# Kernel optimization log

Hardware: AMD Instinct MI355X
Metric: run time of the kernel (lower is better)

## Reference

```python
import jax, jax.numpy as jnp
import numpy as np

IN_FEATURES = 4096
OUT_FEATURES = 8192
LUT_SIZE = 65536  # 256 * 256 two-level codebook


def setup_inputs() -> dict:
    key = jax.random.key(0)
    k_x, k_b, k_f, k_s, k_l = jax.random.split(key, 5)
    x = jax.random.normal(k_x, (2, 256, IN_FEATURES), dtype=jnp.float32)
    base_idx = jax.random.randint(k_b, (OUT_FEATURES, IN_FEATURES), 0, 256, dtype=jnp.int32)
    fine_idx = jax.random.randint(k_f, (OUT_FEATURES, IN_FEATURES), 0, 256, dtype=jnp.int32)
    scale = jax.random.uniform(k_s, (OUT_FEATURES, 1), dtype=jnp.float32)
    lut = jax.random.normal(k_l, (LUT_SIZE,), dtype=jnp.float32)
    return {"x": x, "base_idx": base_idx, "fine_idx": fine_idx, "scale": scale, "lut": lut}


def reference(x, base_idx, fine_idx, scale, lut):
    # Two-level LUT dequant: combined 16-bit index = base*256 + fine
    combined_idx = base_idx * 256 + fine_idx              # [out, in] int32
    weights = lut[combined_idx] * scale                   # [out, in] fp32, per-row scale
    # F.linear(x, weights) == x @ weights.T
    return jnp.einsum('bsi,oi->bso', x, weights)
```

## Files before the change

kernel.cpp:

```cpp
#include <hip/hip_runtime.h>

typedef unsigned short ushort_t;
typedef unsigned int   uint32;
typedef __attribute__((ext_vector_type(8)))  short short8;
typedef __attribute__((ext_vector_type(4)))  float floatx4;
typedef __attribute__((ext_vector_type(16))) float floatx16;

#define IN_F   4096
#define OUT_F  8192
#define M_TOT  512

__device__ __forceinline__ ushort_t f2bf(float f) {
    uint32 u = __builtin_bit_cast(uint32, f);
    u += 0x7FFFu + ((u >> 16) & 1u);
    return (ushort_t)(u >> 16);
}
__device__ __forceinline__ uint32 pack2bf(float a, float b) {
    return (uint32)f2bf(a) | ((uint32)f2bf(b) << 16);
}

__global__ void cvt_x_kernel(const float* __restrict__ x, ushort_t* __restrict__ xb) {
    int i = (blockIdx.x * 256 + threadIdx.x) * 8;
    float4 v0 = *(const float4*)(x + i);
    float4 v1 = *(const float4*)(x + i + 4);
    short8 s;
    s[0] = (short)f2bf(v0.x); s[1] = (short)f2bf(v0.y);
    s[2] = (short)f2bf(v0.z); s[3] = (short)f2bf(v0.w);
    s[4] = (short)f2bf(v1.x); s[5] = (short)f2bf(v1.y);
    s[6] = (short)f2bf(v1.z); s[7] = (short)f2bf(v1.w);
    *(short8*)(xb + i) = s;
}

__global__ __launch_bounds__(1024, 4)
void dequant_kernel(const int* __restrict__ base_idx, const int* __restrict__ fine_idx,
                    const float* __restrict__ lut, ushort_t* __restrict__ wq)
{
    __shared__ ushort_t sh_lut[65536];
    const int tid = threadIdx.x;
    for (int i = tid * 4; i < 65536; i += 1024 * 4) {
        float4 v = *(const float4*)(lut + i);
        *(uint32*)&sh_lut[i]     = pack2bf(v.x, v.y);
        *(uint32*)&sh_lut[i + 2] = pack2bf(v.z, v.w);
    }

    const int row   = blockIdx.x * 32 + (tid >> 5);
    const int kbase = blockIdx.y * 2048 + (tid & 31) * 4;
    const int* bp = base_idx + (size_t)row * IN_F + kbase;
    const int* fp = fine_idx + (size_t)row * IN_F + kbase;
    ushort_t*  op = wq       + (size_t)row * IN_F + kbase;

    int4 cb[2][4], cf[2][4];
#pragma unroll
    for (int u = 0; u < 4; ++u) {
        cb[0][u] = *(const int4*)(bp + u * 128);
        cf[0][u] = *(const int4*)(fp + u * 128);
    }
#pragma unroll
    for (int u = 0; u < 4; ++u) {
        cb[1][u] = *(const int4*)(bp + (4 + u) * 128);
        cf[1][u] = *(const int4*)(fp + (4 + u) * 128);
    }
    __syncthreads();

#pragma unroll
    for (int b = 0; b < 4; ++b) {
        const int cur = b & 1;
#pragma unroll
        for (int u = 0; u < 4; ++u) {
            uint32 w0 = (uint32)sh_lut[(cb[cur][u].x << 8) + cf[cur][u].x]
                      | ((uint32)sh_lut[(cb[cur][u].y << 8) + cf[cur][u].y] << 16);
            uint32 w1 = (uint32)sh_lut[(cb[cur][u].z << 8) + cf[cur][u].z]
                      | ((uint32)sh_lut[(cb[cur][u].w << 8) + cf[cur][u].w] << 16);
            uint2 wv; wv.x = w0; wv.y = w1;
            *(uint2*)(op + (size_t)(b * 4 + u) * 128) = wv;
        }
        if (b + 2 < 4) {
#pragma unroll
            for (int u = 0; u < 4; ++u) {
                cb[cur][u] = *(const int4*)(bp + ((b + 2) * 4 + u) * 128);
                cf[cur][u] = *(const int4*)(fp + ((b + 2) * 4 + u) * 128);
            }
        }
    }
}

#define BK 128
__global__ __launch_bounds__(256, 2)
void gemm_split_kernel(const ushort_t* __restrict__ xb, const ushort_t* __restrict__ wq,
                       float* __restrict__ part)
{
    __shared__ ushort_t shA[128 * BK];
    __shared__ ushort_t shB[128 * BK];

    const int tid  = threadIdx.x;
    const int wave = tid >> 6;
    const int m0   = blockIdx.x * 128;
    const int n0   = blockIdx.y * 128;
    const int kz   = blockIdx.z * (IN_F / 2);

    const int g = (tid & 15) ^ ((tid >> 4) & 7);
    const ushort_t* aBase = xb + (size_t)(m0 + (tid >> 4)) * IN_F + kz + g * 8;
    const ushort_t* bBase = wq + (size_t)(n0 + (tid >> 4)) * IN_F + kz + g * 8;
    typedef __attribute__((address_space(3))) ushort_t lds_us;
    typedef const __attribute__((address_space(1))) void gvoid;
    lds_us* sA3 = (lds_us*)shA;
    lds_us* sB3 = (lds_us*)shB;

    const int lane = tid & 63;
    const int l31  = lane & 31;
    const int lhi  = lane >> 5;
    const int qm   = wave & 1;
    const int qn   = wave >> 1;
    const int rx   = l31 & 7;

    floatx16 acc[2][2];
    const floatx16 z16 = {0.f,0.f,0.f,0.f,0.f,0.f,0.f,0.f,0.f,0.f,0.f,0.f,0.f,0.f,0.f,0.f};
    acc[0][0] = z16; acc[0][1] = z16; acc[1][0] = z16; acc[1][1] = z16;

    for (int kb = 0; kb < IN_F / 2; kb += BK) {
#pragma unroll
        for (int i = 0; i < 8; ++i) {
            __builtin_amdgcn_global_load_lds((gvoid*)(aBase + (size_t)i * 16 * IN_F + kb),
                (__attribute__((address_space(3))) void*)(sA3 + i * 2048 + wave * 512),
                16, 0, 0);
            __builtin_amdgcn_global_load_lds((gvoid*)(bBase + (size_t)i * 16 * IN_F + kb),
                (__attribute__((address_space(3))) void*)(sB3 + i * 2048 + wave * 512),
                16, 0, 0);
        }
        __syncthreads();

#pragma unroll
        for (int ks = 0; ks < 8; ++ks) {
            const int p = ((2 * ks + lhi) ^ rx) * 8;
            short8 a0 = *(const short8*)&shA[(qm * 64 +      l31) * BK + p];
            short8 a1 = *(const short8*)&shA[(qm * 64 + 32 + l31) * BK + p];
            short8 b0 = *(const short8*)&shB[(qn * 64 +      l31) * BK + p];
            short8 b1 = *(const short8*)&shB[(qn * 64 + 32 + l31) * BK + p];
            acc[0][0] = __builtin_amdgcn_mfma_f32_32x32x16_bf16(a0, b0, acc[0][0], 0, 0, 0);
            acc[0][1] = __builtin_amdgcn_mfma_f32_32x32x16_bf16(a0, b1, acc[0][1], 0, 0, 0);
            acc[1][0] = __builtin_amdgcn_mfma_f32_32x32x16_bf16(a1, b0, acc[1][0], 0, 0, 0);
            acc[1][1] = __builtin_amdgcn_mfma_f32_32x32x16_bf16(a1, b1, acc[1][1], 0, 0, 0);
        }
        __syncthreads();
    }

    float* pz = part + (size_t)blockIdx.z * M_TOT * OUT_F;
#pragma unroll
    for (int nt = 0; nt < 2; ++nt) {
        const int col = n0 + qn * 64 + nt * 32 + l31;
#pragma unroll
        for (int mt = 0; mt < 2; ++mt) {
            const int rbase = m0 + qm * 64 + mt * 32 + 4 * lhi;
#pragma unroll
            for (int reg = 0; reg < 16; ++reg) {
                const int row = rbase + (reg & 3) + 8 * (reg >> 2);
                pz[(size_t)row * OUT_F + col] = acc[mt][nt][reg];
            }
        }
    }
}

__global__ void reduce_kernel(const float* __restrict__ p0, const float* __restrict__ p1,
                              const float* __restrict__ scale, float* __restrict__ out)
{
    const int i = (blockIdx.x * 256 + threadIdx.x) * 4;
    float4 a = *(const float4*)(p0 + i);
    float4 b = *(const float4*)(p1 + i);
    float4 s = *(const float4*)(scale + (i & (OUT_F - 1)));
    float4 r;
    r.x = (a.x + b.x) * s.x;
    r.y = (a.y + b.y) * s.y;
    r.z = (a.z + b.z) * s.z;
    r.w = (a.w + b.w) * s.w;
    *(float4*)(out + i) = r;
}

__global__ __launch_bounds__(256)
void gemm_full_kernel(const ushort_t* __restrict__ xb, const ushort_t* __restrict__ wq,
                      const float* __restrict__ scale, float* __restrict__ out)
{
    __shared__ ushort_t shA[128 * BK];
    __shared__ ushort_t shB[128 * BK];

    const int tid  = threadIdx.x;
    const int wave = tid >> 6;
    const int m0   = blockIdx.x * 128;
    const int n0   = blockIdx.y * 128;

    const int g = (tid & 15) ^ ((tid >> 4) & 7);
    const ushort_t* aBase = xb + (size_t)(m0 + (tid >> 4)) * IN_F + g * 8;
    const ushort_t* bBase = wq + (size_t)(n0 + (tid >> 4)) * IN_F + g * 8;
    typedef __attribute__((address_space(3))) ushort_t lds_us;
    typedef const __attribute__((address_space(1))) void gvoid;
    lds_us* sA3 = (lds_us*)shA;
    lds_us* sB3 = (lds_us*)shB;

    const int lane = tid & 63;
    const int l31  = lane & 31;
    const int lhi  = lane >> 5;
    const int qm   = wave & 1;
    const int qn   = wave >> 1;
    const int rx   = l31 & 7;

    floatx16 acc[2][2];
    const floatx16 z16 = {0.f,0.f,0.f,0.f,0.f,0.f,0.f,0.f,0.f,0.f,0.f,0.f,0.f,0.f,0.f,0.f};
    acc[0][0] = z16; acc[0][1] = z16; acc[1][0] = z16; acc[1][1] = z16;

    for (int kb = 0; kb < IN_F; kb += BK) {
#pragma unroll
        for (int i = 0; i < 8; ++i) {
            __builtin_amdgcn_global_load_lds((gvoid*)(aBase + (size_t)i * 16 * IN_F + kb),
                (__attribute__((address_space(3))) void*)(sA3 + i * 2048 + wave * 512), 16, 0, 0);
            __builtin_amdgcn_global_load_lds((gvoid*)(bBase + (size_t)i * 16 * IN_F + kb),
                (__attribute__((address_space(3))) void*)(sB3 + i * 2048 + wave * 512), 16, 0, 0);
        }
        __syncthreads();
#pragma unroll
        for (int ks = 0; ks < 8; ++ks) {
            const int p = ((2 * ks + lhi) ^ rx) * 8;
            short8 a0 = *(const short8*)&shA[(qm * 64 +      l31) * BK + p];
            short8 a1 = *(const short8*)&shA[(qm * 64 + 32 + l31) * BK + p];
            short8 b0 = *(const short8*)&shB[(qn * 64 +      l31) * BK + p];
            short8 b1 = *(const short8*)&shB[(qn * 64 + 32 + l31) * BK + p];
            acc[0][0] = __builtin_amdgcn_mfma_f32_32x32x16_bf16(a0, b0, acc[0][0], 0, 0, 0);
            acc[0][1] = __builtin_amdgcn_mfma_f32_32x32x16_bf16(a0, b1, acc[0][1], 0, 0, 0);
            acc[1][0] = __builtin_amdgcn_mfma_f32_32x32x16_bf16(a1, b0, acc[1][0], 0, 0, 0);
            acc[1][1] = __builtin_amdgcn_mfma_f32_32x32x16_bf16(a1, b1, acc[1][1], 0, 0, 0);
        }
        __syncthreads();
    }
#pragma unroll
    for (int nt = 0; nt < 2; ++nt) {
        const int col = n0 + qn * 64 + nt * 32 + l31;
        const float sc = scale[col];
#pragma unroll
        for (int mt = 0; mt < 2; ++mt) {
            const int rbase = m0 + qm * 64 + mt * 32 + 4 * lhi;
#pragma unroll
            for (int reg = 0; reg < 16; ++reg) {
                const int row = rbase + (reg & 3) + 8 * (reg >> 2);
                out[(size_t)row * OUT_F + col] = acc[mt][nt][reg] * sc;
            }
        }
    }
}

#define NB  32
#define FBK 128
#define WS  136
#define NITER (IN_F / FBK)
template<bool XBF16>
__global__ __launch_bounds__(1024, 4)
void ghost_kernel(const float* __restrict__ xf, const ushort_t* __restrict__ xb,
                  const int* __restrict__ base_idx, const int* __restrict__ fine_idx,
                  const float* __restrict__ scale, const float* __restrict__ lut,
                  float* __restrict__ out)
{
    __shared__ ushort_t sh_lut[65536];
    __shared__ ushort_t sh_w[2][NB * WS];
    const int tid = threadIdx.x;
    const int n0  = blockIdx.x * NB;
    for (int i = tid * 4; i < 65536; i += 1024 * 4) {
        float4 v = *(const float4*)(lut + i);
        sh_lut[i + 0] = f2bf(v.x); sh_lut[i + 1] = f2bf(v.y);
        sh_lut[i + 2] = f2bf(v.z); sh_lut[i + 3] = f2bf(v.w);
    }
    const int sn  = tid >> 5;
    const int skq = (tid & 31) * 4;
    const int* bp = base_idx + (size_t)(n0 + sn) * IN_F + skq;
    const int* fp = fine_idx + (size_t)(n0 + sn) * IN_F + skq;
    __syncthreads();
    int4 pb = *(const int4*)(bp);
    int4 pf = *(const int4*)(fp);
    {
        uint32 w0 = (uint32)sh_lut[(pb.x << 8) + pf.x] | ((uint32)sh_lut[(pb.y << 8) + pf.y] << 16);
        uint32 w1 = (uint32)sh_lut[(pb.z << 8) + pf.z] | ((uint32)sh_lut[(pb.w << 8) + pf.w] << 16);
        uint2 wv; wv.x = w0; wv.y = w1;
        *(uint2*)&sh_w[0][sn * WS + skq] = wv;
    }
    pb = *(const int4*)(bp + FBK);
    pf = *(const int4*)(fp + FBK);
    __syncthreads();
    const int lane = tid & 63;
    const int wave = tid >> 6;
    const int l16  = lane & 15;
    const int quad = lane >> 4;
    floatx4 acc[2][2];
    const floatx4 zero = {0.f, 0.f, 0.f, 0.f};
    acc[0][0] = zero; acc[0][1] = zero; acc[1][0] = zero; acc[1][1] = zero;
    const int mrow = wave * 32 + l16;
    const ushort_t* xrow  = XBF16 ? (xb + (size_t)mrow * IN_F + quad * 8) : (const ushort_t*)nullptr;
    const float*    xrowf = XBF16 ? (const float*)nullptr : (xf + (size_t)mrow * IN_F + quad * 8);
    for (int t = 0; t < NITER; ++t) {
        const int k0 = t * FBK;
        {
            uint32 w0 = (uint32)sh_lut[(pb.x << 8) + pf.x] | ((uint32)sh_lut[(pb.y << 8) + pf.y] << 16);
            uint32 w1 = (uint32)sh_lut[(pb.z << 8) + pf.z] | ((uint32)sh_lut[(pb.w << 8) + pf.w] << 16);
            uint2 wv; wv.x = w0; wv.y = w1;
            *(uint2*)&sh_w[(t + 1) & 1][sn * WS + skq] = wv;
        }
        {
            const int kk = (t + 2 < NITER ? t + 2 : NITER - 1) * FBK;
            pb = *(const int4*)(bp + kk);
            pf = *(const int4*)(fp + kk);
        }
        const ushort_t* wb = sh_w[t & 1];
#pragma unroll
        for (int ks = 0; ks < 4; ++ks) {
            const int kk = k0 + ks * 32;
            short8 b0 = *(const short8*)&wb[l16        * WS + ks * 32 + quad * 8];
            short8 b1 = *(const short8*)&wb[(16 + l16) * WS + ks * 32 + quad * 8];
            short8 a0, a1;
            if (XBF16) {
                a0 = *(const short8*)(xrow + kk);
                a1 = *(const short8*)(xrow + (size_t)16 * IN_F + kk);
            } else {
                const float* p0 = xrowf + kk;
                const float* p1 = xrowf + (size_t)16 * IN_F + kk;
                float4 u0 = *(const float4*)p0, u1 = *(const float4*)(p0 + 4);
                float4 v0 = *(const float4*)p1, v1 = *(const float4*)(p1 + 4);
                a0[0] = (short)f2bf(u0.x); a0[1] = (short)f2bf(u0.y);
                a0[2] = (short)f2bf(u0.z); a0[3] = (short)f2bf(u0.w);
                a0[4] = (short)f2bf(u1.x); a0[5] = (short)f2bf(u1.y);
                a0[6] = (short)f2bf(u1.z); a0[7] = (short)f2bf(u1.w);
                a1[0] = (short)f2bf(v0.x); a1[1] = (short)f2bf(v0.y);
                a1[2] = (short)f2bf(v0.z); a1[3] = (short)f2bf(v0.w);
                a1[4] = (short)f2bf(v1.x); a1[5] = (short)f2bf(v1.y);
                a1[6] = (short)f2bf(v1.z); a1[7] = (short)f2bf(v1.w);
            }
            acc[0][0] = __builtin_amdgcn_mfma_f32_16x16x32_bf16(a0, b0, acc[0][0], 0, 0, 0);
            acc[0][1] = __builtin_amdgcn_mfma_f32_16x16x32_bf16(a0, b1, acc[0][1], 0, 0, 0);
            acc[1][0] = __builtin_amdgcn_mfma_f32_16x16x32_bf16(a1, b0, acc[1][0], 0, 0, 0);
            acc[1][1] = __builtin_amdgcn_mfma_f32_16x16x32_bf16(a1, b1, acc[1][1], 0, 0, 0);
        }
        __syncthreads();
    }
#pragma unroll
    for (int nf = 0; nf < 2; ++nf) {
        const int col = n0 + nf * 16 + l16;
        const float sc = scale[col];
#pragma unroll
        for (int f = 0; f < 2; ++f) {
            const int r0 = wave * 32 + f * 16 + quad * 4;
#pragma unroll
            for (int r = 0; r < 4; ++r) {
                out[(size_t)(r0 + r) * OUT_F + col] = acc[f][nf][r] * sc;
            }
        }
    }
}

extern "C" void kernel_launch(void* const* d_in, const int* in_sizes, int n_in,
                              void* d_out, int out_size, void* d_ws, size_t ws_size,
                              hipStream_t stream) {
    const float* x      = (const float*)d_in[0];
    const int*   bidx   = (const int*)d_in[1];
    const int*   fidx   = (const int*)d_in[2];
    const float* scale  = (const float*)d_in[3];
    const float* lut    = (const float*)d_in[4];
    float*       out    = (float*)d_out;

    const size_t xb_bytes = (size_t)M_TOT * IN_F * sizeof(ushort_t);
    const size_t wq_bytes = (size_t)OUT_F * IN_F * sizeof(ushort_t);
    const size_t pt_bytes = (size_t)M_TOT * OUT_F * sizeof(float);

    if (ws_size >= xb_bytes + wq_bytes + 2 * pt_bytes) {
        ushort_t* xbuf = (ushort_t*)d_ws;
        ushort_t* wbuf = (ushort_t*)((char*)d_ws + xb_bytes);
        float*    part = (float*)((char*)d_ws + xb_bytes + wq_bytes);
        cvt_x_kernel<<<1024, 256, 0, stream>>>(x, xbuf);
        dequant_kernel<<<dim3(256, 2), 1024, 0, stream>>>(bidx, fidx, lut, wbuf);
        gemm_split_kernel<<<dim3(4, 64, 2), 256, 0, stream>>>(xbuf, wbuf, part);
        reduce_kernel<<<(M_TOT * OUT_F) / (256 * 4), 256, 0, stream>>>(
            part, part + (size_t)M_TOT * OUT_F, scale, out);
    } else if (ws_size >= xb_bytes + wq_bytes) {
        ushort_t* xbuf = (ushort_t*)d_ws;
        ushort_t* wbuf = (ushort_t*)((char*)d_ws + xb_bytes);
        cvt_x_kernel<<<1024, 256, 0, stream>>>(x, xbuf);
        dequant_kernel<<<dim3(256, 2), 1024, 0, stream>>>(bidx, fidx, lut, wbuf);
        gemm_full_kernel<<<dim3(4, 64), 256, 0, stream>>>(xbuf, wbuf, scale, out);
    } else if (ws_size >= xb_bytes) {
        ushort_t* xbuf = (ushort_t*)d_ws;
        cvt_x_kernel<<<1024, 256, 0, stream>>>(x, xbuf);
        ghost_kernel<true><<<OUT_F / NB, 1024, 0, stream>>>(x, xbuf, bidx, fidx, scale, lut, out);
    } else {
        ghost_kernel<false><<<OUT_F / NB, 1024, 0, stream>>>(x, nullptr, bidx, fidx, scale, lut, out);
    }
}
```

Baseline: 364.7 us.

## Pre-convert LUT to bf16 once and restructure dequant to full-row blocks

Adds a small kernel that converts the fp32 LUT to bf16 once into workspace, so each dequant block copies the 128KB bf16 table into shared memory instead of reading and converting 256KB of fp32 per block. The dequant grid now covers full rows with one block per 32 rows, halving the number of LUT loads, and each thread handles 8 contiguous indices with a 4-deep software prefetch pipeline and 16-byte stores. The cost is an extra kernel launch and more index registers held per thread.

```diff
diff --git a/kernel.cpp b/kernel.cpp
--- a/kernel.cpp
+++ b/kernel.cpp
@@ -31,56 +31,69 @@
     *(short8*)(xb + i) = s;
 }
 
-__global__ __launch_bounds__(1024, 4)
+__global__ void cvt_lut_kernel(const float* __restrict__ lut, ushort_t* __restrict__ lutb) {
+    int i = (blockIdx.x * 256 + threadIdx.x) * 4;
+    float4 v = *(const float4*)(lut + i);
+    *(uint32*)&lutb[i]     = pack2bf(v.x, v.y);
+    *(uint32*)&lutb[i + 2] = pack2bf(v.z, v.w);
+}
+
+template<bool PRE>
+__global__ __launch_bounds__(1024)
 void dequant_kernel(const int* __restrict__ base_idx, const int* __restrict__ fine_idx,
-                    const float* __restrict__ lut, ushort_t* __restrict__ wq)
+                    const void* __restrict__ lut_src, ushort_t* __restrict__ wq)
 {
     __shared__ ushort_t sh_lut[65536];
     const int tid = threadIdx.x;
-    for (int i = tid * 4; i < 65536; i += 1024 * 4) {
-        float4 v = *(const float4*)(lut + i);
-        *(uint32*)&sh_lut[i]     = pack2bf(v.x, v.y);
-        *(uint32*)&sh_lut[i + 2] = pack2bf(v.z, v.w);
-    }
-
-    const int row   = blockIdx.x * 32 + (tid >> 5);
-    const int kbase = blockIdx.y * 2048 + (tid & 31) * 4;
-    const int* bp = base_idx + (size_t)row * IN_F + kbase;
-    const int* fp = fine_idx + (size_t)row * IN_F + kbase;
-    ushort_t*  op = wq       + (size_t)row * IN_F + kbase;
-
-    int4 cb[2][4], cf[2][4];
-#pragma unroll
-    for (int u = 0; u < 4; ++u) {
-        cb[0][u] = *(const int4*)(bp + u * 128);
-        cf[0][u] = *(const int4*)(fp + u * 128);
-    }
-#pragma unroll
-    for (int u = 0; u < 4; ++u) {
-        cb[1][u] = *(const int4*)(bp + (4 + u) * 128);
-        cf[1][u] = *(const int4*)(fp + (4 + u) * 128);
+    if (PRE) {
+        const ushort_t* lb = (const ushort_t*)lut_src;
+#pragma unroll
+        for (int i = 0; i < 8; ++i) {
+            const int o = (tid + i * 1024) * 8;
+            *(short8*)&sh_lut[o] = *(const short8*)(lb + o);
+        }
+    } else {
+        const float* lf = (const float*)lut_src;
+        for (int i = tid * 4; i < 65536; i += 1024 * 4) {
+            float4 v = *(const float4*)(lf + i);
+            *(uint32*)&sh_lut[i]     = pack2bf(v.x, v.y);
+            *(uint32*)&sh_lut[i + 2] = pack2bf(v.z, v.w);
+        }
+    }
+
+    const int row = blockIdx.x * 32 + (tid >> 5);
+    const int kq  = (tid & 31) * 8;
+    const int* bp = base_idx + (size_t)row * IN_F + kq;
+    const int* fp = fine_idx + (size_t)row * IN_F + kq;
+    ushort_t*  op = wq       + (size_t)row * IN_F + kq;
+
+    int4 rb[4][2], rf[4][2];
+#pragma unroll
+    for (int c = 0; c < 4; ++c) {
+        rb[c][0] = *(const int4*)(bp + c * 256);
+        rb[c][1] = *(const int4*)(bp + c * 256 + 4);
+        rf[c][0] = *(const int4*)(fp + c * 256);
+        rf[c][1] = *(const int4*)(fp + c * 256 + 4);
     }
     __syncthreads();
 
 #pragma unroll
-    for (int b = 0; b < 4; ++b) {
-        const int cur = b & 1;
-#pragma unroll
-        for (int u = 0; u < 4; ++u) {
-            uint32 w0 = (uint32)sh_lut[(cb[cur][u].x << 8) + cf[cur][u].x]
-                      | ((uint32)sh_lut[(cb[cur][u].y << 8) + cf[cur][u].y] << 16);
-            uint32 w1 = (uint32)sh_lut[(cb[cur][u].z << 8) + cf[cur][u].z]
-                      | ((uint32)sh_lut[(cb[cur][u].w << 8) + cf[cur][u].w] << 16);
-            uint2 wv; wv.x = w0; wv.y = w1;
-            *(uint2*)(op + (size_t)(b * 4 + u) * 128) = wv;
-        }
-        if (b + 2 < 4) {
-#pragma unroll
-            for (int u = 0; u < 4; ++u) {
-                cb[cur][u] = *(const int4*)(bp + ((b + 2) * 4 + u) * 128);
-                cf[cur][u] = *(const int4*)(fp + ((b + 2) * 4 + u) * 128);
-            }
-        }
+    for (int c = 0; c < 16; ++c) {
+        const int s = c & 3;
+        const int4 b0 = rb[s][0], b1 = rb[s][1];
+        const int4 f0 = rf[s][0], f1 = rf[s][1];
+        if (c + 4 < 16) {
+            rb[s][0] = *(const int4*)(bp + (c + 4) * 256);
+            rb[s][1] = *(const int4*)(bp + (c + 4) * 256 + 4);
+            rf[s][0] = *(const int4*)(fp + (c + 4) * 256);
+            rf[s][1] = *(const int4*)(fp + (c + 4) * 256 + 4);
+        }
+        uint32 w0 = (uint32)sh_lut[(b0.x << 8) + f0.x] | ((uint32)sh_lut[(b0.y << 8) + f0.y] << 16);
+        uint32 w1 = (uint32)sh_lut[(b0.z << 8) + f0.z] | ((uint32)sh_lut[(b0.w << 8) + f0.w] << 16);
+        uint32 w2 = (uint32)sh_lut[(b1.x << 8) + f1.x] | ((uint32)sh_lut[(b1.y << 8) + f1.y] << 16);
+        uint32 w3 = (uint32)sh_lut[(b1.z << 8) + f1.z] | ((uint32)sh_lut[(b1.w << 8) + f1.w] << 16);
+        uint4 wv; wv.x = w0; wv.y = w1; wv.z = w2; wv.w = w3;
+        *(uint4*)(op + (size_t)c * 256) = wv;
     }
 }
 
@@ -360,16 +373,28 @@
     const float* lut    = (const float*)d_in[4];
     float*       out    = (float*)d_out;
 
-    const size_t xb_bytes = (size_t)M_TOT * IN_F * sizeof(ushort_t);
-    const size_t wq_bytes = (size_t)OUT_F * IN_F * sizeof(ushort_t);
-    const size_t pt_bytes = (size_t)M_TOT * OUT_F * sizeof(float);
-
-    if (ws_size >= xb_bytes + wq_bytes + 2 * pt_bytes) {
+    const size_t xb_bytes  = (size_t)M_TOT * IN_F * sizeof(ushort_t);
+    const size_t wq_bytes  = (size_t)OUT_F * IN_F * sizeof(ushort_t);
+    const size_t pt_bytes  = (size_t)M_TOT * OUT_F * sizeof(float);
+    const size_t lut_bytes = (size_t)65536 * sizeof(ushort_t);
+
+    if (ws_size >= xb_bytes + wq_bytes + 2 * pt_bytes + lut_bytes) {
+        ushort_t* xbuf = (ushort_t*)d_ws;
+        ushort_t* wbuf = (ushort_t*)((char*)d_ws + xb_bytes);
+        float*    part = (float*)((char*)d_ws + xb_bytes + wq_bytes);
+        ushort_t* lbuf = (ushort_t*)((char*)d_ws + xb_bytes + wq_bytes + 2 * pt_bytes);
+        cvt_lut_kernel<<<64, 256, 0, stream>>>(lut, lbuf);
+        cvt_x_kernel<<<1024, 256, 0, stream>>>(x, xbuf);
+        dequant_kernel<true><<<OUT_F / 32, 1024, 0, stream>>>(bidx, fidx, lbuf, wbuf);
+        gemm_split_kernel<<<dim3(4, 64, 2), 256, 0, stream>>>(xbuf, wbuf, part);
+        reduce_kernel<<<(M_TOT * OUT_F) / (256 * 4), 256, 0, stream>>>(
+            part, part + (size_t)M_TOT * OUT_F, scale, out);
+    } else if (ws_size >= xb_bytes + wq_bytes + 2 * pt_bytes) {
         ushort_t* xbuf = (ushort_t*)d_ws;
         ushort_t* wbuf = (ushort_t*)((char*)d_ws + xb_bytes);
         float*    part = (float*)((char*)d_ws + xb_bytes + wq_bytes);
         cvt_x_kernel<<<1024, 256, 0, stream>>>(x, xbuf);
-        dequant_kernel<<<dim3(256, 2), 1024, 0, stream>>>(bidx, fidx, lut, wbuf);
+        dequant_kernel<false><<<OUT_F / 32, 1024, 0, stream>>>(bidx, fidx, lut, wbuf);
         gemm_split_kernel<<<dim3(4, 64, 2), 256, 0, stream>>>(xbuf, wbuf, part);
         reduce_kernel<<<(M_TOT * OUT_F) / (256 * 4), 256, 0, stream>>>(
             part, part + (size_t)M_TOT * OUT_F, scale, out);
@@ -377,7 +402,7 @@
         ushort_t* xbuf = (ushort_t*)d_ws;
         ushort_t* wbuf = (ushort_t*)((char*)d_ws + xb_bytes);
         cvt_x_kernel<<<1024, 256, 0, stream>>>(x, xbuf);
-        dequant_kernel<<<dim3(256, 2), 1024, 0, stream>>>(bidx, fidx, lut, wbuf);
+        dequant_kernel<false><<<OUT_F / 32, 1024, 0, stream>>>(bidx, fidx, lut, wbuf);
         gemm_full_kernel<<<dim3(4, 64), 256, 0, stream>>>(xbuf, wbuf, scale, out);
     } else if (ws_size >= xb_bytes) {
         ushort_t* xbuf = (ushort_t*)d_ws;
```

Result: no change. 367.6 us (+0.8%).
